# Performance work log

Hardware: AMD Instinct MI355X
Metric: run time of the kernel (lower is better)

## Reference

```python
import jax, jax.numpy as jnp
import numpy as np

B, S, I, H = 64, 512, 1024, 1024


def setup_inputs() -> dict:
    key = jax.random.key(0)
    ks = jax.random.split(key, 7)
    sc = 0.02
    return {
        "x": jax.random.normal(ks[0], (B, S, I), jnp.float32),
        "Wx0": jax.random.normal(ks[1], (I, 4 * H), jnp.float32) * sc,
        "Wh0": jax.random.normal(ks[2], (H, 4 * H), jnp.float32) * sc,
        "b0": jax.random.normal(ks[3], (4 * H,), jnp.float32) * sc,
        "Wx1": jax.random.normal(ks[4], (H, 4 * H), jnp.float32) * sc,
        "Wh1": jax.random.normal(ks[5], (H, 4 * H), jnp.float32) * sc,
        "b1": jax.random.normal(ks[6], (4 * H,), jnp.float32) * sc,
    }


def _lstm_layer(x_seq, Wx, Wh, b):
    """x_seq: (S, B, in). Gate order along 4H axis: i, f, g, o."""
    hid = Wh.shape[0]
    # Precompute input-side projections for all timesteps (one big GEMM).
    xg = jnp.einsum('sbi,ih->sbh', x_seq, Wx) + b  # (S, B, 4H)

    def step(carry, xg_t):
        h, c = carry
        g = xg_t + h @ Wh                      # (B, 4H)
        i, f, gg, o = jnp.split(g, 4, axis=-1)
        i = jax.nn.sigmoid(i)
        f = jax.nn.sigmoid(f)
        gg = jnp.tanh(gg)
        o = jax.nn.sigmoid(o)
        c = f * c + i * gg
        h = o * jnp.tanh(c)
        return (h, c), h

    bsz = x_seq.shape[1]
    h0 = jnp.zeros((bsz, hid), x_seq.dtype)
    c0 = jnp.zeros((bsz, hid), x_seq.dtype)
    (_, _), hs = jax.lax.scan(step, (h0, c0), xg)
    return hs  # (S, B, H)


def reference(x, Wx0, Wh0, b0, Wx1, Wh1, b1):
    # batch_first=True -> (B,S,I); internal layout is time-major (S,B,I)
    xs = jnp.swapaxes(x, 0, 1)
    h1 = _lstm_layer(xs, Wx0, Wh0, b0)
    h2 = _lstm_layer(h1, Wx1, Wh1, b1)
    return jnp.swapaxes(h2, 0, 1)  # (B, S, H)
```

## Files before the change

### kernel.cpp

```cpp
#include <hip/hip_runtime.h>
#include <hip/hip_bf16.h>

#define SEQ  512
#define HID  1024
#define G4   4096
#define NBLK 128

typedef short bf16x8 __attribute__((ext_vector_type(8)));
typedef float f32x4  __attribute__((ext_vector_type(4)));
typedef unsigned long long u64;

static __device__ __forceinline__ unsigned short f2b(float f) {
  union { float f; unsigned u; } v; v.f = f;
  unsigned r = (v.u + 0x7FFFu + ((v.u >> 16) & 1u)) >> 16;
  return (unsigned short)r;
}
static __device__ __forceinline__ float b2f_lo(unsigned u) {
  union { unsigned u; float f; } v; v.u = u << 16; return v.f;
}
static __device__ __forceinline__ float b2f_hi(unsigned u) {
  union { unsigned u; float f; } v; v.u = u & 0xFFFF0000u; return v.f;
}

__global__ __launch_bounds__(256) void k_castx(const float* __restrict__ x,
                                               unsigned short* __restrict__ xb) {
  int idx = blockIdx.x * 256 + threadIdx.x;
  int r = idx >> 8, kq = idx & 255;
  int b = r & 63, s = r >> 6;
  float4 v = *reinterpret_cast<const float4*>(x + ((size_t)b * SEQ + s) * HID + (size_t)kq * 4);
  ushort4 o;
  o.x = f2b(v.x); o.y = f2b(v.y); o.z = f2b(v.z); o.w = f2b(v.w);
  *reinterpret_cast<ushort4*>(xb + (size_t)r * HID + kq * 4) = o;
}

__global__ __launch_bounds__(256) void k_wtrans(const float* __restrict__ W,
                                                unsigned short* __restrict__ WT) {
  __shared__ float tls[32][33];
  int tile = blockIdx.x;
  int nt = tile & 127, kt = tile >> 7;
  int tx = threadIdx.x & 31, ty = threadIdx.x >> 5;
  int k0 = kt * 32, n0 = nt * 32;
  for (int i = 0; i < 4; ++i)
    tls[ty + 8 * i][tx] = W[(size_t)(k0 + ty + 8 * i) * G4 + n0 + tx];
  __syncthreads();
  for (int i = 0; i < 4; ++i)
    WT[(size_t)(n0 + ty + 8 * i) * HID + k0 + tx] = f2b(tls[tx][ty + 8 * i]);
}

static __device__ __forceinline__ void poll32(unsigned* row, unsigned tgt) {
  unsigned* p = row + (threadIdx.x & 31);
  long sp = 0;
  for (;;) {
    unsigned v = __hip_atomic_load(p, __ATOMIC_RELAXED, __HIP_MEMORY_SCOPE_AGENT);
    if (__all(v >= tgt)) break;
    if (++sp > 3000000L) break;
  }
  asm volatile("" ::: "memory");
}

__global__ __launch_bounds__(512, 1) void k_scan2(
    const unsigned short* __restrict__ xb,
    const unsigned short* __restrict__ WxT0, const unsigned short* __restrict__ WhT0,
    const float* __restrict__ b0,
    const unsigned short* __restrict__ WxT1, const unsigned short* __restrict__ WhT1,
    const float* __restrict__ b1,
    unsigned short* __restrict__ h1,
    unsigned short* __restrict__ h2, int h2mod,
    float* __restrict__ out,
    unsigned* __restrict__ bars) {
  __shared__ unsigned short wlds[32 * 2048];
  __shared__ float x_lds[2][4][8][64];

  const int bk  = blockIdx.x;
  const int layer = bk >> 7;
  const int nb  = bk & 127;
  const int tid = threadIdx.x;
  const int w   = tid >> 6;
  const int l   = tid & 63;
  const int lq  = l >> 4, lr = l & 15;
  const int rt  = w & 3;
  const bool is_h = (w >= 4);

  const unsigned short* WxT = layer ? WxT1 : WxT0;
  const unsigned short* WhT = layer ? WhT1 : WhT0;
  const float* bias = layer ? b1 : b0;
  const unsigned short* aseq = layer ? h1 : xb;
  unsigned short* hout = layer ? h2 : h1;
  const int hmod = layer ? h2mod : 512;
  float* fout = layer ? out : nullptr;
  unsigned* frow_l0 = bars + rt * 128;
  unsigned* frow_own = bars + (layer * 4 + rt) * 128;
  unsigned* myflag = frow_own + nb;

  {
    int c = tid >> 4, seg = tid & 15;
    int gate = c >> 3, nl = c & 7;
    int gcol = gate * 1024 + nb * 8 + nl;
    const unsigned short* sx = WxT + (size_t)gcol * HID;
    const unsigned short* sh = WhT + (size_t)gcol * HID;
    for (int j = 0; j < 16; ++j) {
      int kk = seg * 128 + j * 8;
      const unsigned short* src = (kk < 1024) ? (sx + kk) : (sh + kk - 1024);
      uint4 v = *reinterpret_cast<const uint4*>(src);
      int db = (c * 4096 + kk * 2) ^ ((c & 7) << 4);
      *reinterpret_cast<uint4*>(reinterpret_cast<char*>(wlds) + db) = v;
    }
  }

  char* wbase = reinterpret_cast<char*>(wlds);
  const int csw = (lr & 7) << 4;
  const int cb0 = (lr) * 4096 + lq * 16;
  const int cb1 = (16 + lr) * 4096 + lq * 16;

  float bias_c[2];
#pragma unroll
  for (int ct = 0; ct < 2; ++ct) {
    int col = ct * 16 + lr;
    bias_c[ct] = bias[(col >> 3) * 1024 + nb * 8 + (col & 7)];
  }

  float cst[4] = {0.f, 0.f, 0.f, 0.f};

  __syncthreads();
  if (is_h) __builtin_amdgcn_s_setprio(1);

  if (!is_h) {
    const bf16x8* ax = reinterpret_cast<const bf16x8*>(aseq) + (size_t)(rt * 16 + lr) * 128 + lq;
    f32x4 acc[2][4] = {};
#pragma unroll
    for (int c = 0; c < 4; ++c) {
      if (layer) poll32(frow_l0 + c * 32, 1u);
#pragma unroll
      for (int ks = c * 8; ks < c * 8 + 8; ++ks) {
        bf16x8 a  = ax[ks * 4];
        bf16x8 bb0 = *reinterpret_cast<const bf16x8*>(wbase + ((cb0 + ks * 64) ^ csw));
        bf16x8 bb1 = *reinterpret_cast<const bf16x8*>(wbase + ((cb1 + ks * 64) ^ csw));
        acc[0][ks & 3] = __builtin_amdgcn_mfma_f32_16x16x32_bf16(a, bb0, acc[0][ks & 3], 0, 0, 0);
        acc[1][ks & 3] = __builtin_amdgcn_mfma_f32_16x16x32_bf16(a, bb1, acc[1][ks & 3], 0, 0, 0);
      }
    }
#pragma unroll
    for (int ct = 0; ct < 2; ++ct) {
      f32x4 s = (acc[ct][0] + acc[ct][1]) + (acc[ct][2] + acc[ct][3]);
      float bc = bias_c[ct];
      x_lds[0][w][ct * 4 + 0][l] = s.x + bc;
      x_lds[0][w][ct * 4 + 1][l] = s.y + bc;
      x_lds[0][w][ct * 4 + 2][l] = s.z + bc;
      x_lds[0][w][ct * 4 + 3][l] = s.w + bc;
    }
  }
  __syncthreads();

  for (int t = 0; t < SEQ; ++t) {
    if (!is_h) {
      if (t + 1 < SEQ) {
        const bf16x8* ax = reinterpret_cast<const bf16x8*>(aseq)
                           + ((size_t)(t + 1) * 64 + rt * 16 + lr) * 128 + lq;
        f32x4 acc[2][4] = {};
#pragma unroll
        for (int c = 0; c < 4; ++c) {
          if (layer) poll32(frow_l0 + c * 32, (unsigned)(t + 2));
#pragma unroll
          for (int ks = c * 8; ks < c * 8 + 8; ++ks) {
            bf16x8 a  = ax[ks * 4];
            bf16x8 bb0 = *reinterpret_cast<const bf16x8*>(wbase + ((cb0 + ks * 64) ^ csw));
            bf16x8 bb1 = *reinterpret_cast<const bf16x8*>(wbase + ((cb1 + ks * 64) ^ csw));
            acc[0][ks & 3] = __builtin_amdgcn_mfma_f32_16x16x32_bf16(a, bb0, acc[0][ks & 3], 0, 0, 0);
            acc[1][ks & 3] = __builtin_amdgcn_mfma_f32_16x16x32_bf16(a, bb1, acc[1][ks & 3], 0, 0, 0);
          }
        }
        int bn2 = (t + 1) & 1;
#pragma unroll
        for (int ct = 0; ct < 2; ++ct) {
          f32x4 s = (acc[ct][0] + acc[ct][1]) + (acc[ct][2] + acc[ct][3]);
          float bc = bias_c[ct];
          x_lds[bn2][w][ct * 4 + 0][l] = s.x + bc;
          x_lds[bn2][w][ct * 4 + 1][l] = s.y + bc;
          x_lds[bn2][w][ct * 4 + 2][l] = s.z + bc;
          x_lds[bn2][w][ct * 4 + 3][l] = s.w + bc;
        }
      }
      if (fout && t > 0) {
        int tc = t - 1;
        const unsigned* sp32 = reinterpret_cast<const unsigned*>(
            hout + (size_t)(tc % hmod) * (64 * HID)) + (size_t)l * 512 + nb * 4 + rt;
        unsigned pv = (hmod == 4)
            ? __hip_atomic_load(sp32, __ATOMIC_RELAXED, __HIP_MEMORY_SCOPE_AGENT)
            : *sp32;
        *reinterpret_cast<float2*>(fout + (size_t)l * (SEQ * HID) + (size_t)tc * HID
                                   + nb * 8 + rt * 2) = make_float2(b2f_lo(pv), b2f_hi(pv));
      }
    } else {
      const int bn = t & 1;
      f32x4 acc[2][4];
#pragma unroll
      for (int ct = 0; ct < 2; ++ct) {
        acc[ct][0] = f32x4{x_lds[bn][rt][ct * 4 + 0][l], x_lds[bn][rt][ct * 4 + 1][l],
                           x_lds[bn][rt][ct * 4 + 2][l], x_lds[bn][rt][ct * 4 + 3][l]};
        acc[ct][1] = f32x4{0.f, 0.f, 0.f, 0.f};
        acc[ct][2] = f32x4{0.f, 0.f, 0.f, 0.f};
        acc[ct][3] = f32x4{0.f, 0.f, 0.f, 0.f};
      }

      if (t > 0) {
        const size_t hbase = (size_t)((t - 1) % hmod) * (64 * HID) + (size_t)(rt * 16 + lr) * HID;
        if (hmod != 4) {
          const bf16x8* hp = reinterpret_cast<const bf16x8*>(hout + hbase) + lq;
#pragma unroll
          for (int c = 0; c < 4; ++c) {
            poll32(frow_own + c * 32, (unsigned)t);
#pragma unroll
            for (int ks = c * 8; ks < c * 8 + 8; ++ks) {
              bf16x8 a = hp[ks * 4];
              bf16x8 bb0 = *reinterpret_cast<const bf16x8*>(wbase + ((cb0 + 2048 + ks * 64) ^ csw));
              bf16x8 bb1 = *reinterpret_cast<const bf16x8*>(wbase + ((cb1 + 2048 + ks * 64) ^ csw));
              acc[0][ks & 3] = __builtin_amdgcn_mfma_f32_16x16x32_bf16(a, bb0, acc[0][ks & 3], 0, 0, 0);
              acc[1][ks & 3] = __builtin_amdgcn_mfma_f32_16x16x32_bf16(a, bb1, acc[1][ks & 3], 0, 0, 0);
            }
          }
        } else {
          const u64* hp = reinterpret_cast<const u64*>(hout + hbase) + lq * 2;
#pragma unroll
          for (int c = 0; c < 4; ++c) {
            poll32(frow_own + c * 32, (unsigned)t);
#pragma unroll
            for (int ks = c * 8; ks < c * 8 + 8; ++ks) {
              u64 q0 = __hip_atomic_load(hp + ks * 8,     __ATOMIC_RELAXED, __HIP_MEMORY_SCOPE_AGENT);
              u64 q1 = __hip_atomic_load(hp + ks * 8 + 1, __ATOMIC_RELAXED, __HIP_MEMORY_SCOPE_AGENT);
              union { u64 q[2]; bf16x8 v; } u; u.q[0] = q0; u.q[1] = q1;
              bf16x8 bb0 = *reinterpret_cast<const bf16x8*>(wbase + ((cb0 + 2048 + ks * 64) ^ csw));
              bf16x8 bb1 = *reinterpret_cast<const bf16x8*>(wbase + ((cb1 + 2048 + ks * 64) ^ csw));
              acc[0][ks & 3] = __builtin_amdgcn_mfma_f32_16x16x32_bf16(u.v, bb0, acc[0][ks & 3], 0, 0, 0);
              acc[1][ks & 3] = __builtin_amdgcn_mfma_f32_16x16x32_bf16(u.v, bb1, acc[1][ks & 3], 0, 0, 0);
            }
          }
        }
      }

      f32x4 s0 = (acc[0][0] + acc[0][1]) + (acc[0][2] + acc[0][3]);
      f32x4 s1 = (acc[1][0] + acc[1][1]) + (acc[1][2] + acc[1][3]);
      float a0[4] = {s0.x, s0.y, s0.z, s0.w};
      float a1[4] = {s1.x, s1.y, s1.z, s1.w};
      float b0r[4], b1r[4];
#pragma unroll
      for (int r = 0; r < 4; ++r) {
        b0r[r] = __shfl_xor(a0[r], 8, 64);
        b1r[r] = __shfl_xor(a1[r], 8, 64);
      }
      const bool isX = ((l & 8) == 0);
      float hvf[4];
#pragma unroll
      for (int r = 0; r < 4; ++r) {
        float gi = isX ? a0[r] : b0r[r];
        float gf = isX ? b0r[r] : a0[r];
        float gg = isX ? a1[r] : b1r[r];
        float go = isX ? b1r[r] : a1[r];
        float ig = 1.f / (1.f + __expf(-gi));
        float fg = 1.f / (1.f + __expf(-gf));
        float e2 = __expf(2.f * gg);
        float gv = (e2 - 1.f) / (e2 + 1.f);
        float og = 1.f / (1.f + __expf(-go));
        cst[r] = fg * cst[r] + ig * gv;
        float e2c = __expf(2.f * cst[r]);
        hvf[r] = og * (e2c - 1.f) / (e2c + 1.f);
      }
      float hn[4];
#pragma unroll
      for (int r = 0; r < 4; ++r) hn[r] = __shfl_xor(hvf[r], 1, 64);
      const bool ev = ((l & 1) == 0);
      unsigned pk[4];
#pragma unroll
      for (int r = 0; r < 4; ++r) {
        float he = ev ? hvf[r] : hn[r];
        float ho = ev ? hn[r] : hvf[r];
        pk[r] = (unsigned)f2b(he) | ((unsigned)f2b(ho) << 16);
      }
      const int sub = ((l >> 3) & 1) * 2 + (l & 1);
      unsigned pks = sub == 0 ? pk[0] : sub == 1 ? pk[1] : sub == 2 ? pk[2] : pk[3];
      const int row = rt * 16 + lq * 4 + sub;
      const int cp  = (lr & 7) >> 1;
      unsigned* hw = reinterpret_cast<unsigned*>(hout + (size_t)(t % hmod) * (64 * HID))
                     + (size_t)row * 512 + nb * 4 + cp;
      __hip_atomic_store(hw, pks, __ATOMIC_RELAXED, __HIP_MEMORY_SCOPE_AGENT);

      asm volatile("s_waitcnt vmcnt(0)" ::: "memory");
      if (l == 0)
        __hip_atomic_store(myflag, (unsigned)(t + 1), __ATOMIC_RELAXED, __HIP_MEMORY_SCOPE_AGENT);
    }
    __syncthreads();
  }

  if (!is_h && fout) {
    const unsigned* sp32 = reinterpret_cast<const unsigned*>(
        hout + (size_t)(511 % hmod) * (64 * HID)) + (size_t)l * 512 + nb * 4 + rt;
    unsigned pv = (hmod == 4)
        ? __hip_atomic_load(sp32, __ATOMIC_RELAXED, __HIP_MEMORY_SCOPE_AGENT)
        : *sp32;
    *reinterpret_cast<float2*>(fout + (size_t)l * (SEQ * HID) + (size_t)511 * HID
                               + nb * 8 + rt * 2) = make_float2(b2f_lo(pv), b2f_hi(pv));
  }
}

extern "C" void kernel_launch(void* const* d_in, const int* in_sizes, int n_in,
                              void* d_out, int out_size, void* d_ws, size_t ws_size,
                              hipStream_t stream) {
  const float* x   = (const float*)d_in[0];
  const float* Wx0 = (const float*)d_in[1];
  const float* Wh0 = (const float*)d_in[2];
  const float* b0  = (const float*)d_in[3];
  const float* Wx1 = (const float*)d_in[4];
  const float* Wh1 = (const float*)d_in[5];
  const float* b1  = (const float*)d_in[6];
  float* out = (float*)d_out;
  char* ws = (char*)d_ws;

  unsigned short* xb   = (unsigned short*)(ws);
  unsigned short* h1   = (unsigned short*)(ws + 67108864);
  unsigned short* WxT0 = (unsigned short*)(ws + 134217728);
  unsigned short* WhT0 = (unsigned short*)(ws + 142606336);
  unsigned short* WxT1 = (unsigned short*)(ws + 150994944);
  unsigned short* WhT1 = (unsigned short*)(ws + 159383552);
  unsigned* bars       = (unsigned*)(ws + 167772160);
  unsigned short* h2   = (unsigned short*)(ws + 167804928);
  int h2mod = (ws_size >= (size_t)167804928 + 67108864) ? 512 : 4;

  hipMemsetAsync(bars, 0, 32768, stream);
  k_castx<<<32768, 256, 0, stream>>>(x, xb);
  k_wtrans<<<4096, 256, 0, stream>>>(Wx0, WxT0);
  k_wtrans<<<4096, 256, 0, stream>>>(Wh0, WhT0);
  k_wtrans<<<4096, 256, 0, stream>>>(Wx1, WxT1);
  k_wtrans<<<4096, 256, 0, stream>>>(Wh1, WhT1);
  k_scan2<<<2 * NBLK, 512, 0, stream>>>(xb, WxT0, WhT0, b0, WxT1, WhT1, b1,
                                        h1, h2, h2mod, out, bars);
}
```

Baseline: 5.574 ms.

## Replace flag barriers with tagged h-ring entries and intra-block sequence counters

Each hidden-state word now carries its timestep tag in a 64-bit store to an 8-slot ring buffer. Consumers spin on the tags directly, with a software-pipelined load/verify/MMA loop, instead of polling per-block flag rows. The per-step __syncthreads between the x-projection and recurrent waves is replaced by LDS sequence counters, and layer 0 is throttled against layer 1's progress so the small ring is not overwritten. This is meant to remove global flag round trips and block-wide barriers from the serial critical path. The cost is doubled h traffic from the tags and extra spin loads, and correctness now depends on ring back-pressure and bounded spins.

Result: slower. 17.60 ms (+215.7%).

```diff
diff --git a/kernel.cpp b/kernel.cpp
--- a/kernel.cpp
+++ b/kernel.cpp
@@ -5,6 +5,8 @@
 #define HID  1024
 #define G4   4096
 #define NBLK 128
+#define RD   8
+#define SLOT 32768
 
 typedef short bf16x8 __attribute__((ext_vector_type(8)));
 typedef float f32x4  __attribute__((ext_vector_type(4)));
@@ -20,6 +22,9 @@
 }
 static __device__ __forceinline__ float b2f_hi(unsigned u) {
   union { unsigned u; float f; } v; v.u = u & 0xFFFF0000u; return v.f;
+}
+static __device__ __forceinline__ u64 gld(const u64* p) {
+  return __hip_atomic_load(p, __ATOMIC_RELAXED, __HIP_MEMORY_SCOPE_AGENT);
 }
 
 __global__ __launch_bounds__(256) void k_castx(const float* __restrict__ x,
@@ -47,15 +52,16 @@
     WT[(size_t)(n0 + ty + 8 * i) * HID + k0 + tx] = f2b(tls[tx][ty + 8 * i]);
 }
 
-static __device__ __forceinline__ void poll32(unsigned* row, unsigned tgt) {
-  unsigned* p = row + (threadIdx.x & 31);
+static __device__ __forceinline__ void seq_wait(unsigned* p, unsigned tgt) {
   long sp = 0;
-  for (;;) {
-    unsigned v = __hip_atomic_load(p, __ATOMIC_RELAXED, __HIP_MEMORY_SCOPE_AGENT);
-    if (__all(v >= tgt)) break;
-    if (++sp > 3000000L) break;
+  while (__hip_atomic_load(p, __ATOMIC_ACQUIRE, __HIP_MEMORY_SCOPE_WORKGROUP) < tgt) {
+    if (++sp > 20000000L) break;
   }
-  asm volatile("" ::: "memory");
+}
+static __device__ __forceinline__ void seq_pub(unsigned* p, unsigned v, int lane) {
+  asm volatile("s_waitcnt lgkmcnt(0)" ::: "memory");
+  if (lane == 0)
+    __hip_atomic_store(p, v, __ATOMIC_RELAXED, __HIP_MEMORY_SCOPE_WORKGROUP);
 }
 
 __global__ __launch_bounds__(512, 1) void k_scan2(
@@ -64,12 +70,12 @@
     const float* __restrict__ b0,
     const unsigned short* __restrict__ WxT1, const unsigned short* __restrict__ WhT1,
     const float* __restrict__ b1,
-    unsigned short* __restrict__ h1,
-    unsigned short* __restrict__ h2, int h2mod,
-    float* __restrict__ out,
-    unsigned* __restrict__ bars) {
+    u64* __restrict__ h1t, u64* __restrict__ h2t,
+    unsigned* __restrict__ prog,
+    float* __restrict__ out) {
   __shared__ unsigned short wlds[32 * 2048];
   __shared__ float x_lds[2][4][8][64];
+  __shared__ unsigned xseq[4], hseq[4];
 
   const int bk  = blockIdx.x;
   const int layer = bk >> 7;
@@ -84,13 +90,10 @@
   const unsigned short* WxT = layer ? WxT1 : WxT0;
   const unsigned short* WhT = layer ? WhT1 : WhT0;
   const float* bias = layer ? b1 : b0;
-  const unsigned short* aseq = layer ? h1 : xb;
-  unsigned short* hout = layer ? h2 : h1;
-  const int hmod = layer ? h2mod : 512;
+  u64* hring = layer ? h2t : h1t;
   float* fout = layer ? out : nullptr;
-  unsigned* frow_l0 = bars + rt * 128;
-  unsigned* frow_own = bars + (layer * 4 + rt) * 128;
-  unsigned* myflag = frow_own + nb;
+
+  if (tid < 4) { xseq[tid] = 0; hseq[tid] = 0; }
 
   {
     int c = tid >> 4, seg = tid & 15;
@@ -121,76 +124,147 @@
 
   float cst[4] = {0.f, 0.f, 0.f, 0.f};
 
-  __syncthreads();
-  if (is_h) __builtin_amdgcn_s_setprio(1);
-
-  if (!is_h) {
-    const bf16x8* ax = reinterpret_cast<const bf16x8*>(aseq) + (size_t)(rt * 16 + lr) * 128 + lq;
-    f32x4 acc[2][4] = {};
-#pragma unroll
-    for (int c = 0; c < 4; ++c) {
-      if (layer) poll32(frow_l0 + c * 32, 1u);
-#pragma unroll
-      for (int ks = c * 8; ks < c * 8 + 8; ++ks) {
-        bf16x8 a  = ax[ks * 4];
-        bf16x8 bb0 = *reinterpret_cast<const bf16x8*>(wbase + ((cb0 + ks * 64) ^ csw));
-        bf16x8 bb1 = *reinterpret_cast<const bf16x8*>(wbase + ((cb1 + ks * 64) ^ csw));
-        acc[0][ks & 3] = __builtin_amdgcn_mfma_f32_16x16x32_bf16(a, bb0, acc[0][ks & 3], 0, 0, 0);
-        acc[1][ks & 3] = __builtin_amdgcn_mfma_f32_16x16x32_bf16(a, bb1, acc[1][ks & 3], 0, 0, 0);
-      }
-    }
+  auto mm_tagged = [&](f32x4 (&acc)[2][4], const u64* rowp, unsigned tag, int koff) {
+    u64 qa[16], qb[16];
+    auto LDG = [&](u64* d, int g) {
+#pragma unroll
+      for (int j = 0; j < 4; ++j)
+#pragma unroll
+        for (int k2 = 0; k2 < 4; ++k2)
+          d[j * 4 + k2] = gld(rowp + (size_t)(g * 4 + j) * 16 + k2);
+    };
+    auto VFY = [&](u64* d, int g) {
+      long sp = 0;
+      for (;;) {
+        bool ok = true;
+#pragma unroll
+        for (int m = 0; m < 16; ++m) ok &= ((unsigned)(d[m] >> 32) == tag);
+        if (ok) break;
+        if (++sp > 60000L) break;
+        LDG(d, g);
+      }
+    };
+    auto MM4 = [&](u64* d, int g) {
+#pragma unroll
+      for (int j = 0; j < 4; ++j) {
+        int ks = g * 4 + j;
+        union { unsigned dw[4]; bf16x8 v; } u;
+        u.dw[0] = (unsigned)d[j * 4 + 0]; u.dw[1] = (unsigned)d[j * 4 + 1];
+        u.dw[2] = (unsigned)d[j * 4 + 2]; u.dw[3] = (unsigned)d[j * 4 + 3];
+        bf16x8 bb0 = *reinterpret_cast<const bf16x8*>(wbase + ((cb0 + koff + ks * 64) ^ csw));
+        bf16x8 bb1 = *reinterpret_cast<const bf16x8*>(wbase + ((cb1 + koff + ks * 64) ^ csw));
+        acc[0][ks & 3] = __builtin_amdgcn_mfma_f32_16x16x32_bf16(u.v, bb0, acc[0][ks & 3], 0, 0, 0);
+        acc[1][ks & 3] = __builtin_amdgcn_mfma_f32_16x16x32_bf16(u.v, bb1, acc[1][ks & 3], 0, 0, 0);
+      }
+    };
+    LDG(qa, 0);
+    LDG(qb, 1); VFY(qa, 0); MM4(qa, 0);
+    LDG(qa, 2); VFY(qb, 1); MM4(qb, 1);
+    LDG(qb, 3); VFY(qa, 2); MM4(qa, 2);
+    LDG(qa, 4); VFY(qb, 3); MM4(qb, 3);
+    LDG(qb, 5); VFY(qa, 4); MM4(qa, 4);
+    LDG(qa, 6); VFY(qb, 5); MM4(qb, 5);
+    LDG(qb, 7); VFY(qa, 6); MM4(qa, 6);
+                VFY(qb, 7); MM4(qb, 7);
+  };
+
+  auto mm_plain = [&](f32x4 (&acc)[2][4], const bf16x8* ap) {
+#pragma unroll 8
+    for (int ks = 0; ks < 32; ++ks) {
+      bf16x8 a  = ap[ks * 4];
+      bf16x8 bb0 = *reinterpret_cast<const bf16x8*>(wbase + ((cb0 + ks * 64) ^ csw));
+      bf16x8 bb1 = *reinterpret_cast<const bf16x8*>(wbase + ((cb1 + ks * 64) ^ csw));
+      acc[0][ks & 3] = __builtin_amdgcn_mfma_f32_16x16x32_bf16(a, bb0, acc[0][ks & 3], 0, 0, 0);
+      acc[1][ks & 3] = __builtin_amdgcn_mfma_f32_16x16x32_bf16(a, bb1, acc[1][ks & 3], 0, 0, 0);
+    }
+  };
+
+  auto store_x = [&](f32x4 (&acc)[2][4], int bufn) {
 #pragma unroll
     for (int ct = 0; ct < 2; ++ct) {
       f32x4 s = (acc[ct][0] + acc[ct][1]) + (acc[ct][2] + acc[ct][3]);
       float bc = bias_c[ct];
-      x_lds[0][w][ct * 4 + 0][l] = s.x + bc;
-      x_lds[0][w][ct * 4 + 1][l] = s.y + bc;
-      x_lds[0][w][ct * 4 + 2][l] = s.z + bc;
-      x_lds[0][w][ct * 4 + 3][l] = s.w + bc;
-    }
-  }
+      x_lds[bufn][w][ct * 4 + 0][l] = s.x + bc;
+      x_lds[bufn][w][ct * 4 + 1][l] = s.y + bc;
+      x_lds[bufn][w][ct * 4 + 2][l] = s.z + bc;
+      x_lds[bufn][w][ct * 4 + 3][l] = s.w + bc;
+    }
+  };
+
   __syncthreads();
-
-  for (int t = 0; t < SEQ; ++t) {
-    if (!is_h) {
+  if (is_h) __builtin_amdgcn_s_setprio(1);
+
+  if (!is_h) {
+    {
+      f32x4 acc[2][4] = {};
+      if (layer) {
+        const u64* rowp = h1t + 0 * SLOT + (size_t)(rt * 16 + lr) * 512 + lq * 4;
+        mm_tagged(acc, rowp, 1u, 0);
+      } else {
+        mm_plain(acc, reinterpret_cast<const bf16x8*>(xb) + (size_t)(rt * 16 + lr) * 128 + lq);
+      }
+      store_x(acc, 0);
+      seq_pub(&xseq[rt], 1u, l);
+    }
+
+    for (int t = 0; t < SEQ; ++t) {
       if (t + 1 < SEQ) {
-        const bf16x8* ax = reinterpret_cast<const bf16x8*>(aseq)
-                           + ((size_t)(t + 1) * 64 + rt * 16 + lr) * 128 + lq;
+        seq_wait(&hseq[rt], (unsigned)t);
         f32x4 acc[2][4] = {};
-#pragma unroll
-        for (int c = 0; c < 4; ++c) {
-          if (layer) poll32(frow_l0 + c * 32, (unsigned)(t + 2));
-#pragma unroll
-          for (int ks = c * 8; ks < c * 8 + 8; ++ks) {
-            bf16x8 a  = ax[ks * 4];
-            bf16x8 bb0 = *reinterpret_cast<const bf16x8*>(wbase + ((cb0 + ks * 64) ^ csw));
-            bf16x8 bb1 = *reinterpret_cast<const bf16x8*>(wbase + ((cb1 + ks * 64) ^ csw));
-            acc[0][ks & 3] = __builtin_amdgcn_mfma_f32_16x16x32_bf16(a, bb0, acc[0][ks & 3], 0, 0, 0);
-            acc[1][ks & 3] = __builtin_amdgcn_mfma_f32_16x16x32_bf16(a, bb1, acc[1][ks & 3], 0, 0, 0);
+        if (layer) {
+          const u64* rowp = h1t + (size_t)((t + 1) % RD) * SLOT
+                            + (size_t)(rt * 16 + lr) * 512 + lq * 4;
+          mm_tagged(acc, rowp, (unsigned)(t + 2), 0);
+        } else {
+          mm_plain(acc, reinterpret_cast<const bf16x8*>(xb)
+                        + ((size_t)(t + 1) * 64 + rt * 16 + lr) * 128 + lq);
+        }
+        store_x(acc, (t + 1) & 1);
+        seq_pub(&xseq[rt], (unsigned)(t + 2), l);
+      }
+      if (layer) {
+        if (t > 0) {
+          const u64* sp = h2t + (size_t)((t - 1) % RD) * SLOT + (size_t)l * 512 + nb * 4 + rt;
+          u64 q; long s2 = 0;
+          do { q = gld(sp); } while ((unsigned)(q >> 32) != (unsigned)t && ++s2 < 60000L);
+          unsigned pv = (unsigned)q;
+          *reinterpret_cast<float2*>(fout + (size_t)l * (SEQ * HID) + (size_t)(t - 1) * HID
+                                     + nb * 8 + rt * 2) = make_float2(b2f_lo(pv), b2f_hi(pv));
+        }
+        if (l == 0)
+          __hip_atomic_store(prog + (nb * 4 + w) * 32, (unsigned)(t + 1),
+                             __ATOMIC_RELAXED, __HIP_MEMORY_SCOPE_AGENT);
+      }
+    }
+
+    if (layer) {
+      const u64* sp = h2t + (size_t)(511 % RD) * SLOT + (size_t)l * 512 + nb * 4 + rt;
+      u64 q; long s2 = 0;
+      do { q = gld(sp); } while ((unsigned)(q >> 32) != 512u && ++s2 < 60000L);
+      unsigned pv = (unsigned)q;
+      *reinterpret_cast<float2*>(fout + (size_t)l * (SEQ * HID) + (size_t)511 * HID
+                                 + nb * 8 + rt * 2) = make_float2(b2f_lo(pv), b2f_hi(pv));
+    }
+  } else {
+    for (int t = 0; t < SEQ; ++t) {
+      if (layer == 0 && t >= RD && (t & 3) == 0) {
+        unsigned tgt = (unsigned)(t - 4);
+        long sp = 0;
+        for (;;) {
+          bool ok = true;
+#pragma unroll
+          for (int j = 0; j < 8; ++j) {
+            unsigned v = __hip_atomic_load(prog + (l * 8 + j) * 32,
+                                           __ATOMIC_RELAXED, __HIP_MEMORY_SCOPE_AGENT);
+            ok &= (v >= tgt);
           }
+          if (__all(ok)) break;
+          if (++sp > 60000L) break;
         }
-        int bn2 = (t + 1) & 1;
-#pragma unroll
-        for (int ct = 0; ct < 2; ++ct) {
-          f32x4 s = (acc[ct][0] + acc[ct][1]) + (acc[ct][2] + acc[ct][3]);
-          float bc = bias_c[ct];
-          x_lds[bn2][w][ct * 4 + 0][l] = s.x + bc;
-          x_lds[bn2][w][ct * 4 + 1][l] = s.y + bc;
-          x_lds[bn2][w][ct * 4 + 2][l] = s.z + bc;
-          x_lds[bn2][w][ct * 4 + 3][l] = s.w + bc;
-        }
-      }
-      if (fout && t > 0) {
-        int tc = t - 1;
-        const unsigned* sp32 = reinterpret_cast<const unsigned*>(
-            hout + (size_t)(tc % hmod) * (64 * HID)) + (size_t)l * 512 + nb * 4 + rt;
-        unsigned pv = (hmod == 4)
-            ? __hip_atomic_load(sp32, __ATOMIC_RELAXED, __HIP_MEMORY_SCOPE_AGENT)
-            : *sp32;
-        *reinterpret_cast<float2*>(fout + (size_t)l * (SEQ * HID) + (size_t)tc * HID
-                                   + nb * 8 + rt * 2) = make_float2(b2f_lo(pv), b2f_hi(pv));
-      }
-    } else {
+        asm volatile("" ::: "memory");
+      }
+
+      seq_wait(&xseq[rt], (unsigned)(t + 1));
       const int bn = t & 1;
       f32x4 acc[2][4];
 #pragma unroll
@@ -201,40 +275,12 @@
         acc[ct][2] = f32x4{0.f, 0.f, 0.f, 0.f};
         acc[ct][3] = f32x4{0.f, 0.f, 0.f, 0.f};
       }
+      seq_pub(&hseq[rt], (unsigned)(t + 1), l);
 
       if (t > 0) {
-        const size_t hbase = (size_t)((t - 1) % hmod) * (64 * HID) + (size_t)(rt * 16 + lr) * HID;
-        if (hmod != 4) {
-          const bf16x8* hp = reinterpret_cast<const bf16x8*>(hout + hbase) + lq;
-#pragma unroll
-          for (int c = 0; c < 4; ++c) {
-            poll32(frow_own + c * 32, (unsigned)t);
-#pragma unroll
-            for (int ks = c * 8; ks < c * 8 + 8; ++ks) {
-              bf16x8 a = hp[ks * 4];
-              bf16x8 bb0 = *reinterpret_cast<const bf16x8*>(wbase + ((cb0 + 2048 + ks * 64) ^ csw));
-              bf16x8 bb1 = *reinterpret_cast<const bf16x8*>(wbase + ((cb1 + 2048 + ks * 64) ^ csw));
-              acc[0][ks & 3] = __builtin_amdgcn_mfma_f32_16x16x32_bf16(a, bb0, acc[0][ks & 3], 0, 0, 0);
-              acc[1][ks & 3] = __builtin_amdgcn_mfma_f32_16x16x32_bf16(a, bb1, acc[1][ks & 3], 0, 0, 0);
-            }
-          }
-        } else {
-          const u64* hp = reinterpret_cast<const u64*>(hout + hbase) + lq * 2;
-#pragma unroll
-          for (int c = 0; c < 4; ++c) {
-            poll32(frow_own + c * 32, (unsigned)t);
-#pragma unroll
-            for (int ks = c * 8; ks < c * 8 + 8; ++ks) {
-              u64 q0 = __hip_atomic_load(hp + ks * 8,     __ATOMIC_RELAXED, __HIP_MEMORY_SCOPE_AGENT);
-              u64 q1 = __hip_atomic_load(hp + ks * 8 + 1, __ATOMIC_RELAXED, __HIP_MEMORY_SCOPE_AGENT);
-              union { u64 q[2]; bf16x8 v; } u; u.q[0] = q0; u.q[1] = q1;
-              bf16x8 bb0 = *reinterpret_cast<const bf16x8*>(wbase + ((cb0 + 2048 + ks * 64) ^ csw));
-              bf16x8 bb1 = *reinterpret_cast<const bf16x8*>(wbase + ((cb1 + 2048 + ks * 64) ^ csw));
-              acc[0][ks & 3] = __builtin_amdgcn_mfma_f32_16x16x32_bf16(u.v, bb0, acc[0][ks & 3], 0, 0, 0);
-              acc[1][ks & 3] = __builtin_amdgcn_mfma_f32_16x16x32_bf16(u.v, bb1, acc[1][ks & 3], 0, 0, 0);
-            }
-          }
-        }
+        const u64* rowp = hring + (size_t)((t - 1) % RD) * SLOT
+                          + (size_t)(rt * 16 + lr) * 512 + lq * 4;
+        mm_tagged(acc, rowp, (unsigned)t, 2048);
       }
 
       f32x4 s0 = (acc[0][0] + acc[0][1]) + (acc[0][2] + acc[0][3]);
@@ -279,25 +325,10 @@
       unsigned pks = sub == 0 ? pk[0] : sub == 1 ? pk[1] : sub == 2 ? pk[2] : pk[3];
       const int row = rt * 16 + lq * 4 + sub;
       const int cp  = (lr & 7) >> 1;
-      unsigned* hw = reinterpret_cast<unsigned*>(hout + (size_t)(t % hmod) * (64 * HID))
-                     + (size_t)row * 512 + nb * 4 + cp;
-      __hip_atomic_store(hw, pks, __ATOMIC_RELAXED, __HIP_MEMORY_SCOPE_AGENT);
-
-      asm volatile("s_waitcnt vmcnt(0)" ::: "memory");
-      if (l == 0)
-        __hip_atomic_store(myflag, (unsigned)(t + 1), __ATOMIC_RELAXED, __HIP_MEMORY_SCOPE_AGENT);
-    }
-    __syncthreads();
-  }
-
-  if (!is_h && fout) {
-    const unsigned* sp32 = reinterpret_cast<const unsigned*>(
-        hout + (size_t)(511 % hmod) * (64 * HID)) + (size_t)l * 512 + nb * 4 + rt;
-    unsigned pv = (hmod == 4)
-        ? __hip_atomic_load(sp32, __ATOMIC_RELAXED, __HIP_MEMORY_SCOPE_AGENT)
-        : *sp32;
-    *reinterpret_cast<float2*>(fout + (size_t)l * (SEQ * HID) + (size_t)511 * HID
-                               + nb * 8 + rt * 2) = make_float2(b2f_lo(pv), b2f_hi(pv));
+      u64 val = ((u64)(unsigned)(t + 1) << 32) | (u64)pks;
+      __hip_atomic_store(hring + (size_t)(t % RD) * SLOT + (size_t)row * 512 + nb * 4 + cp,
+                         val, __ATOMIC_RELAXED, __HIP_MEMORY_SCOPE_AGENT);
+    }
   }
 }
 
@@ -315,21 +346,20 @@
   char* ws = (char*)d_ws;
 
   unsigned short* xb   = (unsigned short*)(ws);
-  unsigned short* h1   = (unsigned short*)(ws + 67108864);
-  unsigned short* WxT0 = (unsigned short*)(ws + 134217728);
-  unsigned short* WhT0 = (unsigned short*)(ws + 142606336);
-  unsigned short* WxT1 = (unsigned short*)(ws + 150994944);
-  unsigned short* WhT1 = (unsigned short*)(ws + 159383552);
-  unsigned* bars       = (unsigned*)(ws + 167772160);
-  unsigned short* h2   = (unsigned short*)(ws + 167804928);
-  int h2mod = (ws_size >= (size_t)167804928 + 67108864) ? 512 : 4;
-
-  hipMemsetAsync(bars, 0, 32768, stream);
+  unsigned short* WxT0 = (unsigned short*)(ws + 67108864);
+  unsigned short* WhT0 = (unsigned short*)(ws + 75497472);
+  unsigned short* WxT1 = (unsigned short*)(ws + 83886080);
+  unsigned short* WhT1 = (unsigned short*)(ws + 92274688);
+  u64* h1t             = (u64*)(ws + 100663296);
+  u64* h2t             = (u64*)(ws + 102760448);
+  unsigned* prog       = (unsigned*)(ws + 104857600);
+
+  hipMemsetAsync(ws + 100663296, 0, 4259840, stream);
   k_castx<<<32768, 256, 0, stream>>>(x, xb);
   k_wtrans<<<4096, 256, 0, stream>>>(Wx0, WxT0);
   k_wtrans<<<4096, 256, 0, stream>>>(Wh0, WhT0);
   k_wtrans<<<4096, 256, 0, stream>>>(Wx1, WxT1);
   k_wtrans<<<4096, 256, 0, stream>>>(Wh1, WhT1);
   k_scan2<<<2 * NBLK, 512, 0, stream>>>(xb, WxT0, WhT0, b0, WxT1, WhT1, b1,
-                                        h1, h2, h2mod, out, bars);
-}
+                                        h1t, h2t, prog, out);
+}
```
